# Kernel optimization log

Measured on AMD Instinct MI355X. Metric: run time of the kernel, lower is better.

Reference implementation:

```python
import jax, jax.numpy as jnp
import numpy as np

LENGTH = 50          # side length of square patch (init kwarg)
HALF = LENGTH // 2   # fill_rectangle uses patch half-sizes around center
FILL_VALUE = 0.0     # fill_mode='constant'


def setup_inputs() -> dict:
    key = jax.random.key(0)
    k_img, k_lab, k_ch, k_cw = jax.random.split(key, 4)
    B, H, W, C = 64, 512, 512, 3
    images = jax.random.normal(k_img, (B, H, W, C), dtype=jnp.float32)
    labels = jax.random.randint(k_lab, (B,), 0, 1000, dtype=jnp.int32)
    center_h = jax.random.randint(k_ch, (B,), 0, H, dtype=jnp.int32)
    center_w = jax.random.randint(k_cw, (B,), 0, W, dtype=jnp.int32)
    return {"images": images, "labels": labels, "center_h": center_h, "center_w": center_w}


def reference(images, labels, center_h, center_w):
    # Vectorized equivalent of tf.map_fn(fill_rectangle, ...):
    # per-sample rectangle [cy-HALF, cy+HALF) x [cx-HALF, cx+HALF),
    # clipped implicitly to image bounds by the index comparisons.
    B, H, W, C = images.shape
    rows = jnp.arange(H)[None, :, None]                # [1, H, 1]
    cols = jnp.arange(W)[None, None, :]                # [1, 1, W]
    ch = center_h[:, None, None]                       # [B, 1, 1]
    cw = center_w[:, None, None]
    mask = ((rows >= ch - HALF) & (rows < ch + HALF) &
            (cols >= cw - HALF) & (cols < cw + HALF))  # [B, H, W]
    out = jnp.where(mask[..., None], jnp.float32(FILL_VALUE), images)
    return out, labels
```

## Files before the change

kernel.cpp:

```cpp
#include <hip/hip_runtime.h>


#define HALF   25
#define BATCH  64
#define IMG_H  512
#define IMG_W  512
#define IMG_C  3
#define N_PIX  (BATCH * IMG_H * IMG_W)
#define N_ELEM ((size_t)N_PIX * IMG_C)
#define N_VEC  (N_ELEM / 4)

__device__ __forceinline__ bool inbox(unsigned p,
                                      const int* __restrict__ ch,
                                      const int* __restrict__ cw) {
    const int w = (int)(p & (IMG_W - 1));
    const int h = (int)((p >> 9) & (IMG_H - 1));
    const int b = (int)(p >> 18);
    const int chb = ch[b];
    const int cwb = cw[b];
    return (h >= chb - HALF) & (h < chb + HALF) &
           (w >= cwb - HALF) & (w < cwb + HALF);
}

__global__ __launch_bounds__(256) void cutout_fused(
    const float4* __restrict__ in,
    float4* __restrict__ out,
    const int* __restrict__ center_h,
    const int* __restrict__ center_w,
    const int* __restrict__ labels,
    float* __restrict__ out_labels)
{
    const unsigned vid = blockIdx.x * 256u + threadIdx.x;

    if (blockIdx.x == 0 && threadIdx.x < BATCH) {
        out_labels[threadIdx.x] = (float)labels[threadIdx.x];
    }

    float4 v = in[vid];

    const unsigned idx4 = vid * 4u;
    const unsigned pi   = idx4 / 3u;
    const unsigned rem  = idx4 - pi * 3u;

    const bool m0 = inbox(pi,     center_h, center_w);
    const bool m1 = inbox(pi + 1, center_h, center_w);

    const bool me0 = m0;
    const bool me1 = (rem >= 2) ? m1 : m0;
    const bool me2 = (rem >= 1) ? m1 : m0;
    const bool me3 = m1;

    if (me0) v.x = 0.0f;
    if (me1) v.y = 0.0f;
    if (me2) v.z = 0.0f;
    if (me3) v.w = 0.0f;

    out[vid] = v;
}

extern "C" void kernel_launch(void* const* d_in, const int* in_sizes, int n_in,
                              void* d_out, int out_size, void* d_ws, size_t ws_size,
                              hipStream_t stream) {
    const float* images   = (const float*)d_in[0];
    const int*   labels   = (const int*)  d_in[1];
    const int*   center_h = (const int*)  d_in[2];
    const int*   center_w = (const int*)  d_in[3];
    float* out = (float*)d_out;

    const unsigned nblocks = N_VEC / 256;
    cutout_fused<<<nblocks, 256, 0, stream>>>(
        (const float4*)images, (float4*)out,
        center_h, center_w, labels, out + N_ELEM);
}
```

Measured before the change: 321.8 us.

## Use 2D grid per image, 4 vectors per thread, fast path and nontemporal stores

Switches to a 2D grid with one image per grid row, so the per-image centers are loaded once per block. Each thread now handles four float4 vectors. Blocks whose row range cannot overlap the cutout rectangle take a pure copy path with no mask math. Output stores use nontemporal hints to reduce cache pollution on this streaming copy, at the cost of fewer blocks and more registers per thread.

```diff
diff --git a/kernel.cpp b/kernel.cpp
--- a/kernel.cpp
+++ b/kernel.cpp
@@ -6,56 +6,89 @@
 #define IMG_H  512
 #define IMG_W  512
 #define IMG_C  3
-#define N_PIX  (BATCH * IMG_H * IMG_W)
-#define N_ELEM ((size_t)N_PIX * IMG_C)
-#define N_VEC  (N_ELEM / 4)
+#define ELEM_PER_IMG (IMG_H * IMG_W * IMG_C)
+#define VEC_PER_IMG  (ELEM_PER_IMG / 4)
+#define VEC_PER_BLOCK 1024
+#define BLOCKS_PER_IMG (VEC_PER_IMG / VEC_PER_BLOCK)
+#define N_ELEM ((size_t)BATCH * ELEM_PER_IMG)
 
-__device__ __forceinline__ bool inbox(unsigned p,
-                                      const int* __restrict__ ch,
-                                      const int* __restrict__ cw) {
-    const int w = (int)(p & (IMG_W - 1));
-    const int h = (int)((p >> 9) & (IMG_H - 1));
-    const int b = (int)(p >> 18);
-    const int chb = ch[b];
-    const int cwb = cw[b];
-    return (h >= chb - HALF) & (h < chb + HALF) &
-           (w >= cwb - HALF) & (w < cwb + HALF);
-}
+typedef float f4 __attribute__((ext_vector_type(4)));
 
 __global__ __launch_bounds__(256) void cutout_fused(
-    const float4* __restrict__ in,
-    float4* __restrict__ out,
+    const f4* __restrict__ in,
+    f4* __restrict__ out,
     const int* __restrict__ center_h,
     const int* __restrict__ center_w,
     const int* __restrict__ labels,
     float* __restrict__ out_labels)
 {
-    const unsigned vid = blockIdx.x * 256u + threadIdx.x;
+    const int b = blockIdx.y;
+    const int chb = center_h[b];
+    const int cwb = center_w[b];
 
-    if (blockIdx.x == 0 && threadIdx.x < BATCH) {
+    if (blockIdx.x == 0 && b == 0 && threadIdx.x < BATCH) {
         out_labels[threadIdx.x] = (float)labels[threadIdx.x];
     }
 
-    float4 v = in[vid];
+    const unsigned vbase_img = blockIdx.x * (unsigned)VEC_PER_BLOCK;
+    const unsigned gvbase    = (unsigned)b * VEC_PER_IMG + vbase_img;
+    const f4* __restrict__ src = in  + gvbase + threadIdx.x;
+    f4*       __restrict__ dst = out + gvbase + threadIdx.x;
 
-    const unsigned idx4 = vid * 4u;
-    const unsigned pi   = idx4 / 3u;
-    const unsigned rem  = idx4 - pi * 3u;
+    const unsigned e0 = vbase_img * 4u;
+    const int r0 = (int)((e0 / 3u) >> 9);
+    const int r1 = (int)(((e0 + 4095u) / 3u) >> 9);
+    const bool overlap = (r1 >= chb - HALF) & (r0 < chb + HALF);
 
-    const bool m0 = inbox(pi,     center_h, center_w);
-    const bool m1 = inbox(pi + 1, center_h, center_w);
+    if (!overlap) {
+        f4 v0 = src[0];
+        f4 v1 = src[256];
+        f4 v2 = src[512];
+        f4 v3 = src[768];
+        __builtin_nontemporal_store(v0, dst);
+        __builtin_nontemporal_store(v1, dst + 256);
+        __builtin_nontemporal_store(v2, dst + 512);
+        __builtin_nontemporal_store(v3, dst + 768);
+        return;
+    }
 
-    const bool me0 = m0;
-    const bool me1 = (rem >= 2) ? m1 : m0;
-    const bool me2 = (rem >= 1) ? m1 : m0;
-    const bool me3 = m1;
+    f4 v0 = src[0];
+    f4 v1 = src[256];
+    f4 v2 = src[512];
+    f4 v3 = src[768];
+    f4 vv[4] = {v0, v1, v2, v3};
 
-    if (me0) v.x = 0.0f;
-    if (me1) v.y = 0.0f;
-    if (me2) v.z = 0.0f;
-    if (me3) v.w = 0.0f;
+    #pragma unroll
+    for (int k = 0; k < 4; ++k) {
+        const unsigned vimg = vbase_img + threadIdx.x + (unsigned)k * 256u;
+        const unsigned idx4 = vimg * 4u;
+        const unsigned pi   = idx4 / 3u;
+        const unsigned rem  = idx4 - pi * 3u;
 
-    out[vid] = v;
+        const unsigned p0 = pi;
+        const unsigned p1 = pi + 1u;
+        const int w0 = (int)(p0 & (IMG_W - 1));
+        const int h0 = (int)(p0 >> 9);
+        const int w1 = (int)(p1 & (IMG_W - 1));
+        const int h1 = (int)(p1 >> 9);
+
+        const bool m0 = (h0 >= chb - HALF) & (h0 < chb + HALF) &
+                        (w0 >= cwb - HALF) & (w0 < cwb + HALF);
+        const bool m1 = (h1 >= chb - HALF) & (h1 < chb + HALF) &
+                        (w1 >= cwb - HALF) & (w1 < cwb + HALF);
+
+        const bool me0 = m0;
+        const bool me1 = (rem >= 2) ? m1 : m0;
+        const bool me2 = (rem >= 1) ? m1 : m0;
+        const bool me3 = m1;
+
+        f4 v = vv[k];
+        if (me0) v[0] = 0.0f;
+        if (me1) v[1] = 0.0f;
+        if (me2) v[2] = 0.0f;
+        if (me3) v[3] = 0.0f;
+        __builtin_nontemporal_store(v, dst + k * 256);
+    }
 }
 
 extern "C" void kernel_launch(void* const* d_in, const int* in_sizes, int n_in,
@@ -67,8 +100,8 @@
     const int*   center_w = (const int*)  d_in[3];
     float* out = (float*)d_out;
 
-    const unsigned nblocks = N_VEC / 256;
-    cutout_fused<<<nblocks, 256, 0, stream>>>(
-        (const float4*)images, (float4*)out,
+    dim3 grid(BLOCKS_PER_IMG, BATCH);
+    cutout_fused<<<grid, 256, 0, stream>>>(
+        (const f4*)images, (f4*)out,
         center_h, center_w, labels, out + N_ELEM);
 }
```

New measurement: 339.2 us. 5.4% more time.

## Copy images with device memcpy and zero only the cutout boxes

Applied to the files above, without the earlier changes.

Replaces the per-element masked copy kernel with a device-to-device memcpy of the whole image tensor, followed by a small kernel that zeroes only the clipped rectangle in each image. This removes the per-element mask computation, the divide-by-3 indexing and the center lookups from the bulk pass, and leaves the bulk copy to the runtime's copy path. In exchange it adds a second launch and a serialized dependency on the stream, and the memcpy may use a copy engine or blit kernel whose throughput can differ from a hand-written streaming kernel.

```diff
diff --git a/kernel.cpp b/kernel.cpp
--- a/kernel.cpp
+++ b/kernel.cpp
@@ -6,56 +6,42 @@
 #define IMG_H  512
 #define IMG_W  512
 #define IMG_C  3
-#define N_PIX  (BATCH * IMG_H * IMG_W)
-#define N_ELEM ((size_t)N_PIX * IMG_C)
-#define N_VEC  (N_ELEM / 4)
+#define ELEM_PER_IMG (IMG_H * IMG_W * IMG_C)
+#define N_ELEM ((size_t)BATCH * ELEM_PER_IMG)
 
-__device__ __forceinline__ bool inbox(unsigned p,
-                                      const int* __restrict__ ch,
-                                      const int* __restrict__ cw) {
-    const int w = (int)(p & (IMG_W - 1));
-    const int h = (int)((p >> 9) & (IMG_H - 1));
-    const int b = (int)(p >> 18);
-    const int chb = ch[b];
-    const int cwb = cw[b];
-    return (h >= chb - HALF) & (h < chb + HALF) &
-           (w >= cwb - HALF) & (w < cwb + HALF);
-}
-
-__global__ __launch_bounds__(256) void cutout_fused(
-    const float4* __restrict__ in,
-    float4* __restrict__ out,
+__global__ __launch_bounds__(256) void zero_boxes(
+    float* __restrict__ out,
     const int* __restrict__ center_h,
     const int* __restrict__ center_w,
     const int* __restrict__ labels,
     float* __restrict__ out_labels)
 {
-    const unsigned vid = blockIdx.x * 256u + threadIdx.x;
+    const int b = blockIdx.x;
 
-    if (blockIdx.x == 0 && threadIdx.x < BATCH) {
+    if (b == 0 && threadIdx.x < BATCH) {
         out_labels[threadIdx.x] = (float)labels[threadIdx.x];
     }
 
-    float4 v = in[vid];
+    const int chb = center_h[b];
+    const int cwb = center_w[b];
 
-    const unsigned idx4 = vid * 4u;
-    const unsigned pi   = idx4 / 3u;
-    const unsigned rem  = idx4 - pi * 3u;
+    const int r0 = max(chb - HALF, 0);
+    const int r1 = min(chb + HALF, IMG_H);
+    const int c0 = max(cwb - HALF, 0);
+    const int c1 = min(cwb + HALF, IMG_W);
 
-    const bool m0 = inbox(pi,     center_h, center_w);
-    const bool m1 = inbox(pi + 1, center_h, center_w);
+    const int row_elems = (c1 - c0) * IMG_C;
+    const int wid  = (int)(threadIdx.x >> 6);
+    const int lane = (int)(threadIdx.x & 63);
 
-    const bool me0 = m0;
-    const bool me1 = (rem >= 2) ? m1 : m0;
-    const bool me2 = (rem >= 1) ? m1 : m0;
-    const bool me3 = m1;
+    float* img = out + (size_t)b * ELEM_PER_IMG;
 
-    if (me0) v.x = 0.0f;
-    if (me1) v.y = 0.0f;
-    if (me2) v.z = 0.0f;
-    if (me3) v.w = 0.0f;
-
-    out[vid] = v;
+    for (int r = r0 + wid; r < r1; r += 4) {
+        float* row = img + ((size_t)r * IMG_W + c0) * IMG_C;
+        for (int i = lane; i < row_elems; i += 64) {
+            row[i] = 0.0f;
+        }
+    }
 }
 
 extern "C" void kernel_launch(void* const* d_in, const int* in_sizes, int n_in,
@@ -67,8 +53,9 @@
     const int*   center_w = (const int*)  d_in[3];
     float* out = (float*)d_out;
 
-    const unsigned nblocks = N_VEC / 256;
-    cutout_fused<<<nblocks, 256, 0, stream>>>(
-        (const float4*)images, (float4*)out,
-        center_h, center_w, labels, out + N_ELEM);
+    hipMemcpyAsync(out, images, N_ELEM * sizeof(float),
+                   hipMemcpyDeviceToDevice, stream);
+
+    zero_boxes<<<BATCH, 256, 0, stream>>>(
+        out, center_h, center_w, labels, out + N_ELEM);
 }
```

Measured after the change: 332.2 us. 1.03x slower.
